# Kernel tuning notes

Hardware: AMD Instinct MI355X
Metric: run time of the kernel (lower is better)

## Reference

```python
import jax, jax.numpy as jnp
import numpy as np

N_NODES = 50000

def setup_inputs() -> dict:
    key = jax.random.key(0)
    ks = jax.random.split(key, 9)
    x = jax.random.normal(ks[0], (N_NODES, 100), dtype=jnp.float32)
    W0 = jax.random.normal(ks[1], (100, 64), dtype=jnp.float32) * (1.0 / np.sqrt(100))
    b0 = jnp.zeros((64,), dtype=jnp.float32)
    W1 = jax.random.normal(ks[2], (64, 64), dtype=jnp.float32) * (1.0 / np.sqrt(64))
    b1 = jnp.zeros((64,), dtype=jnp.float32)
    W2 = jax.random.normal(ks[3], (64, 47), dtype=jnp.float32) * (1.0 / np.sqrt(64))
    b2 = jnp.zeros((47,), dtype=jnp.float32)
    src = jax.random.randint(ks[4], (800000,), 0, N_NODES, dtype=jnp.int64)
    dst = jax.random.randint(ks[5], (800000,), 0, N_NODES, dtype=jnp.int64)
    return {"x": x, "W0": W0, "b0": b0, "W1": W1, "b1": b1,
            "W2": W2, "b2": b2, "src": src, "dst": dst}

def _degree_norms(src, dst, n_nodes):
    ones = jnp.ones(src.shape[0], dtype=jnp.float32)
    deg_out = jax.ops.segment_sum(ones, src, num_segments=n_nodes)
    deg_in = jax.ops.segment_sum(ones, dst, num_segments=n_nodes)
    # DGL GraphConv norm='both': clamp degree to >= 1 then D^{-1/2}
    norm_src = jax.lax.rsqrt(jnp.maximum(deg_out, 1.0))  # [N]
    norm_dst = jax.lax.rsqrt(jnp.maximum(deg_in, 1.0))   # [N]
    return norm_src, norm_dst

def _graph_conv(h, W, b, src, dst, norm_src, norm_dst, n_nodes):
    # h: [N, F_in] -> D_in^{-1/2} A D_out^{-1/2} h W + b
    m = h * norm_src[:, None]                              # [N, F_in]
    agg = jax.ops.segment_sum(m[src], dst, num_segments=n_nodes)  # SpMM gather/scatter
    agg = agg * norm_dst[:, None]
    return agg @ W + b

def reference(x, W0, b0, W1, b1, W2, b2, src, dst):
    n = x.shape[0]
    norm_src, norm_dst = _degree_norms(src, dst, n)
    # dropout is identity in eval mode (deterministic reference)
    h = jax.nn.relu(_graph_conv(x, W0, b0, src, dst, norm_src, norm_dst, n))
    h = jax.nn.relu(_graph_conv(h, W1, b1, src, dst, norm_src, norm_dst, n))
    out = _graph_conv(h, W2, b2, src, dst, norm_src, norm_dst, n)
    return out
```

## Files before the change

### kernel.cpp

```cpp
#include <hip/hip_runtime.h>
#include <stdint.h>


#define NNODES 50000
#define NBW    12500
#define HT     1024
#define EPT    7
#define EPB    (HT * EPT)

__global__ __launch_bounds__(HT) void hist_kernel(
        const int* __restrict__ src, const int* __restrict__ dst,
        unsigned* __restrict__ cnt_dst, unsigned* __restrict__ cnt_src,
        unsigned char* __restrict__ rank, int E) {
    __shared__ unsigned h[NBW];
    const int b = blockIdx.x, base = b * EPB;
    int s[EPT], d[EPT]; bool val[EPT]; unsigned char rk[EPT];
    #pragma unroll
    for (int j = 0; j < EPT; ++j) {
        int e = base + j * HT + (int)threadIdx.x;
        val[j] = (e < E);
        s[j] = val[j] ? src[e] : 0;
        d[j] = val[j] ? dst[e] : 0;
        rk[j] = 0;
    }
    for (int w = threadIdx.x; w < NBW; w += HT) h[w] = 0u;
    __syncthreads();
    #pragma unroll
    for (int j = 0; j < EPT; ++j) if (val[j]) {
        unsigned sh = 8u * (d[j] & 3);
        unsigned old = atomicAdd(&h[d[j] >> 2], 1u << sh);
        rk[j] = (unsigned char)((old >> sh) & 0xffu);
    }
    __syncthreads();
    for (int w = threadIdx.x; w < NBW; w += HT) {
        cnt_dst[(size_t)b * NBW + w] = h[w];
        h[w] = 0u;
    }
    __syncthreads();
    #pragma unroll
    for (int j = 0; j < EPT; ++j) if (val[j])
        atomicAdd(&h[s[j] >> 2], 1u << (8u * (s[j] & 3)));
    #pragma unroll
    for (int j = 0; j < EPT; ++j) {
        int e = base + j * HT + (int)threadIdx.x;
        if (val[j]) rank[e] = rk[j];
    }
    __syncthreads();
    for (int w = threadIdx.x; w < NBW; w += HT)
        cnt_src[(size_t)b * NBW + w] = h[w];
}

__global__ __launch_bounds__(1024) void merge_scan_kernel(
        unsigned* __restrict__ cnt_dst, const unsigned* __restrict__ cnt_src,
        int* __restrict__ row_off, int* __restrict__ blocksum,
        float* __restrict__ ns, float* __restrict__ nd, int hb) {
    const int t = threadIdx.x;
    const int half = t & 511;
    const int w = blockIdx.x * 512 + half;
    const bool is_dst = (t < 512);
    unsigned deg[4] = {0, 0, 0, 0};
    if (w < NBW) {
        if (is_dst) {
            for (int b = 0; b < hb; ++b) {
                unsigned v = cnt_dst[(size_t)b * NBW + w];
                cnt_dst[(size_t)b * NBW + w] =
                    deg[0] | (deg[1] << 8) | (deg[2] << 16) | (deg[3] << 24);
                #pragma unroll
                for (int k = 0; k < 4; ++k) deg[k] += (v >> (8 * k)) & 0xffu;
            }
            #pragma unroll
            for (int k = 0; k < 4; ++k)
                nd[4 * w + k] = rsqrtf((float)(deg[k] < 1u ? 1u : deg[k]));
        } else {
            for (int b = 0; b < hb; ++b) {
                unsigned v = cnt_src[(size_t)b * NBW + w];
                #pragma unroll
                for (int k = 0; k < 4; ++k) deg[k] += (v >> (8 * k)) & 0xffu;
            }
            #pragma unroll
            for (int k = 0; k < 4; ++k)
                ns[4 * w + k] = rsqrtf((float)(deg[k] < 1u ? 1u : deg[k]));
        }
    }
    __shared__ int wsum[8];
    int sum = (is_dst && w < NBW) ? (int)(deg[0] + deg[1] + deg[2] + deg[3]) : 0;
    int lane = t & 63, wv = t >> 6;
    int incl = sum;
    #pragma unroll
    for (int off = 1; off < 64; off <<= 1) {
        int x = __shfl_up(incl, off, 64);
        if (lane >= off) incl += x;
    }
    if (is_dst && lane == 63) wsum[wv] = incl;
    __syncthreads();
    if (t < 8) {
        int v = wsum[t], ic = v;
        #pragma unroll
        for (int off = 1; off < 8; off <<= 1) {
            int x = __shfl_up(ic, off, 8);
            if ((t & 7) >= off) ic += x;
        }
        wsum[t] = ic;
    }
    __syncthreads();
    if (is_dst && w < NBW) {
        int base = (wv > 0 ? wsum[wv - 1] : 0) + incl - sum;
        row_off[4 * w + 0] = base;
        row_off[4 * w + 1] = base + (int)deg[0];
        row_off[4 * w + 2] = base + (int)(deg[0] + deg[1]);
        row_off[4 * w + 3] = base + (int)(deg[0] + deg[1] + deg[2]);
    }
    if (t == 0) blocksum[blockIdx.x] = wsum[7];
}

__global__ void scan2_kernel(const int* __restrict__ blocksum,
                             int* __restrict__ blockoff, int nb) {
    int i = threadIdx.x;
    int v = (i < nb) ? blocksum[i] : 0;
    int incl = v;
    #pragma unroll
    for (int off = 1; off < 64; off <<= 1) {
        int x = __shfl_up(incl, off, 64);
        if (i >= off) incl += x;
    }
    if (i < nb) blockoff[i] = incl - v;
}

__global__ __launch_bounds__(HT) void scatter_kernel(
        const int* __restrict__ src, const int* __restrict__ dst,
        const unsigned* __restrict__ cnt_dst, const int* __restrict__ row_off,
        const int* __restrict__ blockoff, const unsigned char* __restrict__ rank,
        unsigned short* __restrict__ src_sorted, int E) {
    const int b = blockIdx.x, base = b * EPB;
    #pragma unroll
    for (int j = 0; j < EPT; ++j) {
        int e = base + j * HT + (int)threadIdx.x;
        if (e >= E) continue;
        int d = dst[e];
        unsigned pk = cnt_dst[(size_t)b * NBW + (d >> 2)];
        unsigned pfx = (pk >> (8u * (d & 3))) & 0xffu;
        unsigned p = (unsigned)(row_off[d] + blockoff[d >> 11]) + pfx + (unsigned)rank[e];
        src_sorted[p] = (unsigned short)src[e];
    }
}

template <int FIN, int FOUT>
__global__ __launch_bounds__(256) void rowscale_gemm2(const float* __restrict__ H,
        const float* __restrict__ ns, const float* __restrict__ Wg,
        float* __restrict__ T, int n) {
    constexpr int WS = (FOUT + 3) & ~3;
    constexpr int RP = FIN + 4;
    constexpr int Q  = FIN / 4;
    __shared__ __align__(16) float Wlds[FIN * WS];
    __shared__ __align__(16) float rows[64 * RP];

    for (int i = threadIdx.x; i < FIN * WS; i += 256) {
        int k = i / WS, j = i - k * WS;
        Wlds[i] = (j < FOUT) ? Wg[k * FOUT + j] : 0.0f;
    }
    int node0 = blockIdx.x * 64;
    for (int idx = threadIdx.x; idx < 64 * Q; idx += 256) {
        int nl = idx / Q, q = idx - nl * Q;
        int node = node0 + nl;
        float4 v = make_float4(0.f, 0.f, 0.f, 0.f);
        float s = 0.f;
        if (node < n) {
            v = *(const float4*)&H[(size_t)node * FIN + 4 * q];
            s = ns[node];
        }
        float4* d4 = (float4*)&rows[nl * RP + 4 * q];
        d4->x = v.x * s; d4->y = v.y * s; d4->z = v.z * s; d4->w = v.w * s;
    }
    __syncthreads();

    int w = threadIdx.x >> 6;
    int lane = threadIdx.x & 63;
    int g = lane >> 4, f = lane & 15;
    if (4 * f < WS) {
        float4 acc0 = make_float4(0.f,0.f,0.f,0.f), acc1 = acc0, acc2 = acc0, acc3 = acc0;
        const float* r0 = &rows[(w * 16 + 0 * 4 + g) * RP];
        const float* r1 = &rows[(w * 16 + 1 * 4 + g) * RP];
        const float* r2 = &rows[(w * 16 + 2 * 4 + g) * RP];
        const float* r3 = &rows[(w * 16 + 3 * 4 + g) * RP];
        for (int k = 0; k < FIN; ++k) {
            float4 wv = *(const float4*)&Wlds[k * WS + 4 * f];
            float h0 = r0[k], h1 = r1[k], h2 = r2[k], h3 = r3[k];
            acc0.x += h0 * wv.x; acc0.y += h0 * wv.y; acc0.z += h0 * wv.z; acc0.w += h0 * wv.w;
            acc1.x += h1 * wv.x; acc1.y += h1 * wv.y; acc1.z += h1 * wv.z; acc1.w += h1 * wv.w;
            acc2.x += h2 * wv.x; acc2.y += h2 * wv.y; acc2.z += h2 * wv.z; acc2.w += h2 * wv.w;
            acc3.x += h3 * wv.x; acc3.y += h3 * wv.y; acc3.z += h3 * wv.z; acc3.w += h3 * wv.w;
        }
        float4 accs[4] = {acc0, acc1, acc2, acc3};
        #pragma unroll
        for (int r = 0; r < 4; ++r) {
            int node = node0 + w * 16 + r * 4 + g;
            if (node < n)
                *(float4*)&T[(size_t)node * WS + 4 * f] = accs[r];
        }
    }
}

__global__ __launch_bounds__(256) void agg_mid_kernel(const float* __restrict__ T,
        const int* __restrict__ row_off, const int* __restrict__ blockoff,
        const unsigned short* __restrict__ srcs, const float* __restrict__ nd,
        const float* __restrict__ bias, float* __restrict__ H, int n, int E) {
    int node = (blockIdx.x * 256 + threadIdx.x) >> 6;
    int lane = threadIdx.x & 63;
    int g = lane >> 4, f = lane & 15;
    if (node >= n) return;
    int beg = row_off[node] + blockoff[node >> 11];
    int end = (node + 1 < n) ? row_off[node + 1] + blockoff[(node + 1) >> 11] : E;
    float4 acc = make_float4(0.f, 0.f, 0.f, 0.f);
    float4 acc2 = acc;
    int e = beg + g;
    for (; e + 4 < end; e += 8) {
        int s0 = srcs[e], s1 = srcs[e + 4];
        float4 v0 = *(const float4*)&T[(size_t)s0 * 64 + 4 * f];
        float4 v1 = *(const float4*)&T[(size_t)s1 * 64 + 4 * f];
        acc.x  += v0.x; acc.y  += v0.y; acc.z  += v0.z; acc.w  += v0.w;
        acc2.x += v1.x; acc2.y += v1.y; acc2.z += v1.z; acc2.w += v1.w;
    }
    if (e < end) {
        float4 v0 = *(const float4*)&T[(size_t)srcs[e] * 64 + 4 * f];
        acc.x += v0.x; acc.y += v0.y; acc.z += v0.z; acc.w += v0.w;
    }
    acc.x += acc2.x; acc.y += acc2.y; acc.z += acc2.z; acc.w += acc2.w;
    #pragma unroll
    for (int m = 16; m <= 32; m <<= 1) {
        acc.x += __shfl_xor(acc.x, m, 64);
        acc.y += __shfl_xor(acc.y, m, 64);
        acc.z += __shfl_xor(acc.z, m, 64);
        acc.w += __shfl_xor(acc.w, m, 64);
    }
    if (g == 0) {
        float sd = nd[node];
        float4 o;
        o.x = fmaxf(fmaf(acc.x, sd, bias[4 * f + 0]), 0.f);
        o.y = fmaxf(fmaf(acc.y, sd, bias[4 * f + 1]), 0.f);
        o.z = fmaxf(fmaf(acc.z, sd, bias[4 * f + 2]), 0.f);
        o.w = fmaxf(fmaf(acc.w, sd, bias[4 * f + 3]), 0.f);
        *(float4*)&H[(size_t)node * 64 + 4 * f] = o;
    }
}

__global__ __launch_bounds__(256) void agg_final_kernel(const float* __restrict__ T,
        const int* __restrict__ row_off, const int* __restrict__ blockoff,
        const unsigned short* __restrict__ srcs, const float* __restrict__ nd,
        const float* __restrict__ bias, float* __restrict__ Out, int n, int E) {
    int node = (blockIdx.x * 256 + threadIdx.x) >> 6;
    int lane = threadIdx.x & 63;
    int g = lane >> 4, f = lane & 15;
    if (node >= n) return;
    int beg = row_off[node] + blockoff[node >> 11];
    int end = (node + 1 < n) ? row_off[node + 1] + blockoff[(node + 1) >> 11] : E;
    float4 acc = make_float4(0.f, 0.f, 0.f, 0.f);
    float4 acc2 = acc;
    if (f < 12) {
        int e = beg + g;
        for (; e + 4 < end; e += 8) {
            int s0 = srcs[e], s1 = srcs[e + 4];
            float4 v0 = *(const float4*)&T[(size_t)s0 * 48 + 4 * f];
            float4 v1 = *(const float4*)&T[(size_t)s1 * 48 + 4 * f];
            acc.x  += v0.x; acc.y  += v0.y; acc.z  += v0.z; acc.w  += v0.w;
            acc2.x += v1.x; acc2.y += v1.y; acc2.z += v1.z; acc2.w += v1.w;
        }
        if (e < end) {
            float4 v0 = *(const float4*)&T[(size_t)srcs[e] * 48 + 4 * f];
            acc.x += v0.x; acc.y += v0.y; acc.z += v0.z; acc.w += v0.w;
        }
    }
    acc.x += acc2.x; acc.y += acc2.y; acc.z += acc2.z; acc.w += acc2.w;
    #pragma unroll
    for (int m = 16; m <= 32; m <<= 1) {
        acc.x += __shfl_xor(acc.x, m, 64);
        acc.y += __shfl_xor(acc.y, m, 64);
        acc.z += __shfl_xor(acc.z, m, 64);
        acc.w += __shfl_xor(acc.w, m, 64);
    }
    if (g == 0 && f < 12) {
        float sd = nd[node];
        float a[4] = {acc.x, acc.y, acc.z, acc.w};
        #pragma unroll
        for (int j = 0; j < 4; ++j) {
            int c = 4 * f + j;
            if (c < 47)
                Out[(size_t)node * 47 + c] = fmaf(a[j], sd, bias[c]);
        }
    }
}

extern "C" void kernel_launch(void* const* d_in, const int* in_sizes, int n_in,
                              void* d_out, int out_size, void* d_ws, size_t ws_size,
                              hipStream_t stream) {
    const float* x  = (const float*)d_in[0];
    const float* W0 = (const float*)d_in[1];
    const float* b0 = (const float*)d_in[2];
    const float* W1 = (const float*)d_in[3];
    const float* b1 = (const float*)d_in[4];
    const float* W2 = (const float*)d_in[5];
    const float* b2 = (const float*)d_in[6];
    const int* src  = (const int*)d_in[7];
    const int* dst  = (const int*)d_in[8];
    float* out = (float*)d_out;

    const int N = NNODES;
    const int E = in_sizes[7];
    const int hb = (E + EPB - 1) / EPB;
    const int nchunk = (NBW + 511) / 512;

    unsigned* u = (unsigned*)d_ws;
    unsigned* cnt_dst = u;  u += (size_t)hb * NBW;
    unsigned* cnt_src = u;  u += (size_t)hb * NBW;
    int* p = (int*)u;
    int* row_off  = p;  p += N;
    int* blocksum = p;  p += 64;
    int* blockoff = p;  p += 64;
    unsigned char*  rank       = (unsigned char*)p;
    unsigned short* src_sorted = (unsigned short*)(rank + E);
    uintptr_t fp = ((uintptr_t)(src_sorted + E) + 15) & ~(uintptr_t)15;
    float* f = (float*)fp;
    float* norm_src = f;  f += N;
    float* norm_dst = f;  f += N;
    float* h_buf    = f;  f += (size_t)N * 64;
    float* t01      = f;  f += (size_t)N * 64;
    float* t2       = f;  f += (size_t)N * 48;

    hist_kernel<<<hb, HT, 0, stream>>>(src, dst, cnt_dst, cnt_src, rank, E);
    merge_scan_kernel<<<nchunk, 1024, 0, stream>>>(cnt_dst, cnt_src, row_off,
                                                   blocksum, norm_src, norm_dst, hb);
    scan2_kernel<<<1, 64, 0, stream>>>(blocksum, blockoff, nchunk);
    scatter_kernel<<<hb, HT, 0, stream>>>(src, dst, cnt_dst, row_off, blockoff,
                                          rank, src_sorted, E);

    const int gemm_grid = (N + 63) / 64;
    const int agg_grid  = (N * 64 + 255) / 256;

    rowscale_gemm2<100, 64><<<gemm_grid, 256, 0, stream>>>(x, norm_src, W0, t01, N);
    agg_mid_kernel<<<agg_grid, 256, 0, stream>>>(t01, row_off, blockoff, src_sorted,
                                                 norm_dst, b0, h_buf, N, E);
    rowscale_gemm2<64, 64><<<gemm_grid, 256, 0, stream>>>(h_buf, norm_src, W1, t01, N);
    agg_mid_kernel<<<agg_grid, 256, 0, stream>>>(t01, row_off, blockoff, src_sorted,
                                                 norm_dst, b1, h_buf, N, E);
    rowscale_gemm2<64, 47><<<gemm_grid, 256, 0, stream>>>(h_buf, norm_src, W2, t2, N);
    agg_final_kernel<<<agg_grid, 256, 0, stream>>>(t2, row_off, blockoff, src_sorted,
                                                   norm_dst, b2, out, N, E);
}
```

Measured before the change: 227.0 us.

## Store transformed features in fp16 and sort neighbor lists per row

The per-layer transformed feature tables T are now written by the GEMM kernels as packed half precision and widened back to float in the aggregation kernels, which halves the bytes moved by the random neighbor gathers. A new row_sort_kernel runs a per-node bitonic sort over the CSR source indices inside one wavefront, so each node's gathers touch memory in ascending address order and get better cache locality. The trade-offs are fp16 rounding error in the aggregated features and an extra kernel launch. The sort also assumes no row holds more than 64 edges; longer rows would only be partly sorted and would lose their tail entries.

Result: faster. 218.0 us (-4.0%).

```diff
diff --git a/kernel.cpp b/kernel.cpp
--- a/kernel.cpp
+++ b/kernel.cpp
@@ -1,4 +1,5 @@
 #include <hip/hip_runtime.h>
+#include <hip/hip_fp16.h>
 #include <stdint.h>
 
 
@@ -7,6 +8,8 @@
 #define HT     1024
 #define EPT    7
 #define EPB    (HT * EPT)
+
+struct __align__(8) h4pack { __half2 a, b; };
 
 __global__ __launch_bounds__(HT) void hist_kernel(
         const int* __restrict__ src, const int* __restrict__ dst,
@@ -144,10 +147,36 @@
     }
 }
 
+__global__ __launch_bounds__(256) void row_sort_kernel(
+        const int* __restrict__ row_off, const int* __restrict__ blockoff,
+        unsigned short* __restrict__ srcs, int n, int E) {
+    int node = (blockIdx.x * 256 + threadIdx.x) >> 6;
+    int lane = threadIdx.x & 63;
+    if (node >= n) return;
+    int beg = row_off[node] + blockoff[node >> 11];
+    int end = (node + 1 < n) ? row_off[node + 1] + blockoff[(node + 1) >> 11] : E;
+    int len = end - beg;
+    if (len <= 1) return;
+    unsigned v = (lane < len) ? (unsigned)srcs[beg + lane] : 0xffffffffu;
+    #pragma unroll
+    for (int k = 2; k <= 64; k <<= 1) {
+        #pragma unroll
+        for (int j = k >> 1; j >= 1; j >>= 1) {
+            unsigned o = __shfl_xor(v, j, 64);
+            bool down  = (lane & k) != 0;
+            bool lower = (lane & j) == 0;
+            unsigned mn = (v < o) ? v : o;
+            unsigned mx = (v < o) ? o : v;
+            v = (lower != down) ? mn : mx;
+        }
+    }
+    if (lane < len) srcs[beg + lane] = (unsigned short)v;
+}
+
 template <int FIN, int FOUT>
-__global__ __launch_bounds__(256) void rowscale_gemm2(const float* __restrict__ H,
+__global__ __launch_bounds__(256) void rowscale_gemm_h(const float* __restrict__ H,
         const float* __restrict__ ns, const float* __restrict__ Wg,
-        float* __restrict__ T, int n) {
+        __half* __restrict__ T, int n) {
     constexpr int WS = (FOUT + 3) & ~3;
     constexpr int RP = FIN + 4;
     constexpr int Q  = FIN / 4;
@@ -194,13 +223,17 @@
         #pragma unroll
         for (int r = 0; r < 4; ++r) {
             int node = node0 + w * 16 + r * 4 + g;
-            if (node < n)
-                *(float4*)&T[(size_t)node * WS + 4 * f] = accs[r];
-        }
-    }
-}
-
-__global__ __launch_bounds__(256) void agg_mid_kernel(const float* __restrict__ T,
+            if (node < n) {
+                h4pack pk;
+                pk.a = __float22half2_rn(make_float2(accs[r].x, accs[r].y));
+                pk.b = __float22half2_rn(make_float2(accs[r].z, accs[r].w));
+                *(h4pack*)&T[(size_t)node * WS + 4 * f] = pk;
+            }
+        }
+    }
+}
+
+__global__ __launch_bounds__(256) void agg_mid_kernel(const __half* __restrict__ T,
         const int* __restrict__ row_off, const int* __restrict__ blockoff,
         const unsigned short* __restrict__ srcs, const float* __restrict__ nd,
         const float* __restrict__ bias, float* __restrict__ H, int n, int E) {
@@ -215,14 +248,17 @@
     int e = beg + g;
     for (; e + 4 < end; e += 8) {
         int s0 = srcs[e], s1 = srcs[e + 4];
-        float4 v0 = *(const float4*)&T[(size_t)s0 * 64 + 4 * f];
-        float4 v1 = *(const float4*)&T[(size_t)s1 * 64 + 4 * f];
-        acc.x  += v0.x; acc.y  += v0.y; acc.z  += v0.z; acc.w  += v0.w;
-        acc2.x += v1.x; acc2.y += v1.y; acc2.z += v1.z; acc2.w += v1.w;
+        h4pack r0 = *(const h4pack*)&T[(size_t)s0 * 64 + 4 * f];
+        h4pack r1 = *(const h4pack*)&T[(size_t)s1 * 64 + 4 * f];
+        float2 a0 = __half22float2(r0.a), a1 = __half22float2(r0.b);
+        float2 b0 = __half22float2(r1.a), b1 = __half22float2(r1.b);
+        acc.x  += a0.x; acc.y  += a0.y; acc.z  += a1.x; acc.w  += a1.y;
+        acc2.x += b0.x; acc2.y += b0.y; acc2.z += b1.x; acc2.w += b1.y;
     }
     if (e < end) {
-        float4 v0 = *(const float4*)&T[(size_t)srcs[e] * 64 + 4 * f];
-        acc.x += v0.x; acc.y += v0.y; acc.z += v0.z; acc.w += v0.w;
+        h4pack r0 = *(const h4pack*)&T[(size_t)srcs[e] * 64 + 4 * f];
+        float2 a0 = __half22float2(r0.a), a1 = __half22float2(r0.b);
+        acc.x += a0.x; acc.y += a0.y; acc.z += a1.x; acc.w += a1.y;
     }
     acc.x += acc2.x; acc.y += acc2.y; acc.z += acc2.z; acc.w += acc2.w;
     #pragma unroll
@@ -243,7 +279,7 @@
     }
 }
 
-__global__ __launch_bounds__(256) void agg_final_kernel(const float* __restrict__ T,
+__global__ __launch_bounds__(256) void agg_final_kernel(const __half* __restrict__ T,
         const int* __restrict__ row_off, const int* __restrict__ blockoff,
         const unsigned short* __restrict__ srcs, const float* __restrict__ nd,
         const float* __restrict__ bias, float* __restrict__ Out, int n, int E) {
@@ -259,14 +295,17 @@
         int e = beg + g;
         for (; e + 4 < end; e += 8) {
             int s0 = srcs[e], s1 = srcs[e + 4];
-            float4 v0 = *(const float4*)&T[(size_t)s0 * 48 + 4 * f];
-            float4 v1 = *(const float4*)&T[(size_t)s1 * 48 + 4 * f];
-            acc.x  += v0.x; acc.y  += v0.y; acc.z  += v0.z; acc.w  += v0.w;
-            acc2.x += v1.x; acc2.y += v1.y; acc2.z += v1.z; acc2.w += v1.w;
+            h4pack r0 = *(const h4pack*)&T[(size_t)s0 * 48 + 4 * f];
+            h4pack r1 = *(const h4pack*)&T[(size_t)s1 * 48 + 4 * f];
+            float2 a0 = __half22float2(r0.a), a1 = __half22float2(r0.b);
+            float2 b0 = __half22float2(r1.a), b1 = __half22float2(r1.b);
+            acc.x  += a0.x; acc.y  += a0.y; acc.z  += a1.x; acc.w  += a1.y;
+            acc2.x += b0.x; acc2.y += b0.y; acc2.z += b1.x; acc2.w += b1.y;
         }
         if (e < end) {
-            float4 v0 = *(const float4*)&T[(size_t)srcs[e] * 48 + 4 * f];
-            acc.x += v0.x; acc.y += v0.y; acc.z += v0.z; acc.w += v0.w;
+            h4pack r0 = *(const h4pack*)&T[(size_t)srcs[e] * 48 + 4 * f];
+            float2 a0 = __half22float2(r0.a), a1 = __half22float2(r0.b);
+            acc.x += a0.x; acc.y += a0.y; acc.z += a1.x; acc.w += a1.y;
         }
     }
     acc.x += acc2.x; acc.y += acc2.y; acc.z += acc2.z; acc.w += acc2.w;
@@ -322,8 +361,8 @@
     float* norm_src = f;  f += N;
     float* norm_dst = f;  f += N;
     float* h_buf    = f;  f += (size_t)N * 64;
-    float* t01      = f;  f += (size_t)N * 64;
-    float* t2       = f;  f += (size_t)N * 48;
+    __half* t01 = (__half*)f;
+    __half* t2  = t01 + (size_t)N * 64;
 
     hist_kernel<<<hb, HT, 0, stream>>>(src, dst, cnt_dst, cnt_src, rank, E);
     merge_scan_kernel<<<nchunk, 1024, 0, stream>>>(cnt_dst, cnt_src, row_off,
@@ -331,17 +370,19 @@
     scan2_kernel<<<1, 64, 0, stream>>>(blocksum, blockoff, nchunk);
     scatter_kernel<<<hb, HT, 0, stream>>>(src, dst, cnt_dst, row_off, blockoff,
                                           rank, src_sorted, E);
+    row_sort_kernel<<<(NNODES * 64 + 255) / 256, 256, 0, stream>>>(
+        row_off, blockoff, src_sorted, N, E);
 
     const int gemm_grid = (N + 63) / 64;
     const int agg_grid  = (N * 64 + 255) / 256;
 
-    rowscale_gemm2<100, 64><<<gemm_grid, 256, 0, stream>>>(x, norm_src, W0, t01, N);
+    rowscale_gemm_h<100, 64><<<gemm_grid, 256, 0, stream>>>(x, norm_src, W0, t01, N);
     agg_mid_kernel<<<agg_grid, 256, 0, stream>>>(t01, row_off, blockoff, src_sorted,
                                                  norm_dst, b0, h_buf, N, E);
-    rowscale_gemm2<64, 64><<<gemm_grid, 256, 0, stream>>>(h_buf, norm_src, W1, t01, N);
+    rowscale_gemm_h<64, 64><<<gemm_grid, 256, 0, stream>>>(h_buf, norm_src, W1, t01, N);
     agg_mid_kernel<<<agg_grid, 256, 0, stream>>>(t01, row_off, blockoff, src_sorted,
                                                  norm_dst, b1, h_buf, N, E);
-    rowscale_gemm2<64, 47><<<gemm_grid, 256, 0, stream>>>(h_buf, norm_src, W2, t2, N);
+    rowscale_gemm_h<64, 47><<<gemm_grid, 256, 0, stream>>>(h_buf, norm_src, W2, t2, N);
     agg_final_kernel<<<agg_grid, 256, 0, stream>>>(t2, row_off, blockoff, src_sorted,
                                                    norm_dst, b2, out, N, E);
 }
```
